# Kernel tuning notes

Hardware: AMD Instinct MI355X
Metric: run time of the kernel (lower is better)

Reference implementation:

```python
import jax, jax.numpy as jnp
import numpy as np

N_NODES = 100000
N_EDGES = 1600000


def setup_inputs() -> dict:
    key = jax.random.key(0)
    ks = jax.random.split(key, 6)
    x = jax.random.normal(ks[0], (N_NODES, 128), dtype=jnp.float32)
    edge_src = jax.random.randint(ks[1], (N_EDGES,), 0, N_NODES, dtype=jnp.int64)
    edge_dst = jax.random.randint(ks[2], (N_EDGES,), 0, N_NODES, dtype=jnp.int64)
    # GCNConv weights (bias=False); glorot-like scaling
    W1 = jax.random.normal(ks[3], (128, 64), dtype=jnp.float32) * (1.0 / np.sqrt(128))
    W2 = jax.random.normal(ks[4], (64, 64), dtype=jnp.float32) * (1.0 / np.sqrt(64))
    W3 = jax.random.normal(ks[5], (64, 40), dtype=jnp.float32) * (1.0 / np.sqrt(64))
    return {"x": x, "edge_src": edge_src, "edge_dst": edge_dst,
            "W1": W1, "W2": W2, "W3": W3}


def reference(x, edge_src, edge_dst, W1, W2, W3):
    # SGC forward (eval mode: dropout is identity).
    # Each GCNConv(normalize=False, bias=False): out = A @ (h @ W)
    n = x.shape[0]

    def conv(h, W):
        hw = h @ W                      # [N, d_out] dense transform
        msgs = hw[edge_src]             # [E, d_out] gather over edges
        return jax.ops.segment_sum(msgs, edge_dst, num_segments=n)  # scatter-add

    h = conv(x, W1)
    h = conv(h, W2)
    h = conv(h, W3)
    return jax.nn.log_softmax(h, axis=-1)
```

## Files before the change

### kernel.cpp

```cpp
#include <hip/hip_runtime.h>
#include <hip/hip_fp16.h>
#include <math.h>


#define BW    128
#define NBMAX 1024
#define BCAP  3072
#define D     40
#define RS    64
#define NPW   12

typedef unsigned short u16;
typedef unsigned int   u32;

static __device__ inline u32 hadd2u(u32 a, u32 b) {
    __half2 ha = *(__half2*)&a, hb = *(__half2*)&b;
    __half2 r = __hadd2(ha, hb);
    return *(u32*)&r;
}

__global__ void k_w12(const float* __restrict__ W1, const float* __restrict__ W2,
                      float* __restrict__ W12, int* __restrict__ gcnt) {
    int idx = blockIdx.x * blockDim.x + threadIdx.x;
    if (blockIdx.x == 0) {
        for (int i = threadIdx.x; i < NBMAX; i += blockDim.x) gcnt[i] = 0;
    }
    if (idx >= 128 * 64) return;
    int r = idx >> 6, c = idx & 63;
    float acc = 0.f;
#pragma unroll
    for (int k = 0; k < 64; ++k) acc += W1[r * 64 + k] * W2[k * 64 + c];
    W12[idx] = acc;
}

__global__ void k_wc(const float* __restrict__ W12, const float* __restrict__ W3,
                     float* __restrict__ Wc) {
    int idx = blockIdx.x * blockDim.x + threadIdx.x;
    if (idx >= 128 * 40) return;
    int r = idx / 40, c = idx - r * 40;
    float acc = 0.f;
#pragma unroll
    for (int k = 0; k < 64; ++k) acc += W12[r * 64 + k] * W3[k * 40 + c];
    Wc[idx] = acc;
}

__global__ void k_gemm(const float4* __restrict__ x4, const float4* __restrict__ Wc4,
                       u16* __restrict__ yout, int n_nodes) {
    __shared__ float4 wc[128 * 10];
    for (int i = threadIdx.x; i < 1280; i += blockDim.x) wc[i] = Wc4[i];
    __syncthreads();
    int tid = blockIdx.x * blockDim.x + threadIdx.x;
    int node = tid / 5, j0 = tid - node * 5;
    if (node >= n_nodes) return;
    float4 a0 = {0.f, 0.f, 0.f, 0.f}, a1 = {0.f, 0.f, 0.f, 0.f};
    const float4* xr = x4 + (size_t)node * 32;
#pragma unroll
    for (int k4 = 0; k4 < 32; ++k4) {
        float4 v = xr[k4];
#pragma unroll
        for (int kk = 0; kk < 4; ++kk) {
            float c = (kk == 0) ? v.x : (kk == 1) ? v.y : (kk == 2) ? v.z : v.w;
            float4 w0 = wc[(k4 * 4 + kk) * 10 + j0 * 2];
            float4 w1 = wc[(k4 * 4 + kk) * 10 + j0 * 2 + 1];
            a0.x += c * w0.x; a0.y += c * w0.y; a0.z += c * w0.z; a0.w += c * w0.w;
            a1.x += c * w1.x; a1.y += c * w1.y; a1.z += c * w1.z; a1.w += c * w1.w;
        }
    }
    __half2 h0 = __floats2half2_rn(a0.x, a0.y);
    __half2 h1 = __floats2half2_rn(a0.z, a0.w);
    __half2 h2 = __floats2half2_rn(a1.x, a1.y);
    __half2 h3 = __floats2half2_rn(a1.z, a1.w);
    uint4 st;
    st.x = *(u32*)&h0; st.y = *(u32*)&h1; st.z = *(u32*)&h2; st.w = *(u32*)&h3;
    *(uint4*)(yout + (size_t)node * RS + j0 * 8) = st;
}

#define PCHUNK 2048
__global__ void k_part(const int* __restrict__ src, const int* __restrict__ dst,
                       int* __restrict__ gcnt, int* __restrict__ part,
                       int E, int nb) {
    __shared__ int h[NBMAX];
    __shared__ int base[NBMAX];
    int t = threadIdx.x;
    int e0 = blockIdx.x * PCHUNK;
    int e1 = min(e0 + PCHUNK, E);
    for (int i = t; i < nb; i += 256) h[i] = 0;
    __syncthreads();
    for (int e = e0 + t; e < e1; e += 256)
        atomicAdd(&h[dst[e] >> 7], 1);
    __syncthreads();
    for (int i = t; i < nb; i += 256) {
        int c = h[i];
        base[i] = c ? atomicAdd(&gcnt[i], c) : 0;
    }
    __syncthreads();
    for (int i = t; i < nb; i += 256) h[i] = 0;
    __syncthreads();
    for (int e = e0 + t; e < e1; e += 1024) {
        bool v1 = (e + 256) < e1, v2 = (e + 512) < e1, v3 = (e + 768) < e1;
        int d0 = dst[e], s0 = src[e];
        int d1 = v1 ? dst[e + 256] : 0, s1 = v1 ? src[e + 256] : 0;
        int d2 = v2 ? dst[e + 512] : 0, s2 = v2 ? src[e + 512] : 0;
        int d3 = v3 ? dst[e + 768] : 0, s3 = v3 ? src[e + 768] : 0;
        int b0 = d0 >> 7, b1 = d1 >> 7, b2 = d2 >> 7, b3 = d3 >> 7;
        int p0 = base[b0] + atomicAdd(&h[b0], 1);
        int p1 = v1 ? (base[b1] + atomicAdd(&h[b1], 1)) : BCAP;
        int p2 = v2 ? (base[b2] + atomicAdd(&h[b2], 1)) : BCAP;
        int p3 = v3 ? (base[b3] + atomicAdd(&h[b3], 1)) : BCAP;
        if (p0 < BCAP) part[(size_t)b0 * BCAP + p0] = (s0 << 7) | (d0 & 127);
        if (p1 < BCAP) part[(size_t)b1 * BCAP + p1] = (s1 << 7) | (d1 & 127);
        if (p2 < BCAP) part[(size_t)b2 * BCAP + p2] = (s2 << 7) | (d2 & 127);
        if (p3 < BCAP) part[(size_t)b3 * BCAP + p3] = (s3 << 7) | (d3 & 127);
    }
}

__global__ void k_csr(const int* __restrict__ part, const int* __restrict__ gcnt,
                      int* __restrict__ begv, int* __restrict__ endv,
                      int* __restrict__ ssort, int N) {
    __shared__ int cnt[BW];
    __shared__ int pos[BW];
    __shared__ int cur[BW];
    __shared__ int wsum[2];
    int b = blockIdx.x, t = threadIdx.x;
    int m = min(gcnt[b], BCAP);
    const int* bp = part + (size_t)b * BCAP;
    if (t < BW) cnt[t] = 0;
    __syncthreads();
    for (int k = t; k < m; k += 256)
        atomicAdd(&cnt[bp[k] & 127], 1);
    __syncthreads();
    int v = 0, inc = 0;
    if (t < BW) {
        v = cnt[t];
        inc = v;
#pragma unroll
        for (int off = 1; off < 64; off <<= 1) {
            int u = __shfl_up(inc, off, 64);
            if ((t & 63) >= off) inc += u;
        }
        if ((t & 63) == 63) wsum[t >> 6] = inc;
    }
    __syncthreads();
    int node0 = b * BW;
    if (t < BW) {
        int local = ((t >= 64) ? wsum[0] : 0) + inc - v;
        pos[t] = local;
        cur[t] = 0;
        if (node0 + t < N) {
            begv[node0 + t] = b * BCAP + local;
            endv[node0 + t] = b * BCAP + local + v;
        }
    }
    __syncthreads();
    for (int k = t; k < m; k += 256) {
        int p = bp[k];
        int r = p & 127;
        int loc = atomicAdd(&cur[r], 1);
        ssort[(size_t)b * BCAP + pos[r] + loc] = p >> 7;
    }
}

template <int FINAL>
__global__ void k_agg(const u16* __restrict__ yin, void* __restrict__ youtv,
                      const int* __restrict__ begv, const int* __restrict__ endv,
                      const int* __restrict__ srcs, int n_nodes) {
    int wid = (blockIdx.x * blockDim.x + threadIdx.x) >> 6;
    int lane = threadIdx.x & 63;
    int g = lane / 5;
    int sub = lane - g * 5;
    int node = wid * NPW + g;
    bool nv = (g < NPW) && (node < n_nodes);
    int ncl = nv ? node : 0;
    int beg = begv[ncl];
    int deg = nv ? (endv[ncl] - beg) : 0;
    u32 suboff = (u32)sub * 16u;
    u32 c0 = 0, c1 = 0, c2 = 0, c3 = 0;
    for (int k = 0; __any(k < deg); k += 5) {
        int sv = (k + sub < deg) ? srcs[beg + k + sub] : 0;
#pragma unroll
        for (int j = 0; j < 5; ++j) {
            int s = __shfl(sv, g * 5 + j, 64);
            if (k + j < deg) {
                uint4 w = *(const uint4*)((const char*)yin +
                              (size_t)(((u32)s << 7) + suboff));
                c0 = hadd2u(c0, w.x); c1 = hadd2u(c1, w.y);
                c2 = hadd2u(c2, w.z); c3 = hadd2u(c3, w.w);
            }
        }
    }
    if (FINAL) {
        float2 f0 = __half22float2(*(__half2*)&c0);
        float2 f1 = __half22float2(*(__half2*)&c1);
        float2 f2 = __half22float2(*(__half2*)&c2);
        float2 f3 = __half22float2(*(__half2*)&c3);
        int s1 = sub + 1; s1 = (s1 >= 5) ? s1 - 5 : s1;
        int s2 = sub + 2; s2 = (s2 >= 5) ? s2 - 5 : s2;
        int s4 = sub + 4; s4 = (s4 >= 5) ? s4 - 5 : s4;
        int r1 = g * 5 + s1, r2 = g * 5 + s2, r4 = g * 5 + s4;
        float m0 = fmaxf(fmaxf(fmaxf(f0.x, f0.y), fmaxf(f1.x, f1.y)),
                         fmaxf(fmaxf(f2.x, f2.y), fmaxf(f3.x, f3.y)));
        float m = fmaxf(m0, __shfl(m0, r1, 64));
        m = fmaxf(m, __shfl(m, r2, 64));
        m = fmaxf(m, __shfl(m0, r4, 64));
        float e0 = __expf(f0.x - m) + __expf(f0.y - m) + __expf(f1.x - m) +
                   __expf(f1.y - m) + __expf(f2.x - m) + __expf(f2.y - m) +
                   __expf(f3.x - m) + __expf(f3.y - m);
        float sm = e0 + __shfl(e0, r1, 64);
        sm = sm + __shfl(sm, r2, 64);
        sm = sm + __shfl(e0, r4, 64);
        float ls = __logf(sm) + m;
        if (nv) {
            float4 o1 = {f0.x - ls, f0.y - ls, f1.x - ls, f1.y - ls};
            float4 o2 = {f2.x - ls, f2.y - ls, f3.x - ls, f3.y - ls};
            float* op = (float*)youtv + (size_t)node * D + sub * 8;
            *(float4*)op = o1;
            *(float4*)(op + 4) = o2;
        }
    } else {
        if (nv) {
            uint4 st = {c0, c1, c2, c3};
            *(uint4*)((u16*)youtv + (size_t)node * RS + sub * 8) = st;
        }
    }
}

extern "C" void kernel_launch(void* const* d_in, const int* in_sizes, int n_in,
                              void* d_out, int out_size, void* d_ws, size_t ws_size,
                              hipStream_t stream) {
    const float* x   = (const float*)d_in[0];
    const int* esrc  = (const int*)d_in[1];
    const int* edst  = (const int*)d_in[2];
    const float* W1  = (const float*)d_in[3];
    const float* W2  = (const float*)d_in[4];
    const float* W3  = (const float*)d_in[5];
    int N = in_sizes[0] / 128;
    int E = in_sizes[1];
    float* out = (float*)d_out;

    int nb = (N + BW - 1) / BW;

    char* ws = (char*)d_ws;
    auto alloc = [&](size_t bytes) {
        char* p = ws;
        ws += (bytes + 255) & ~(size_t)255;
        return p;
    };
    u16* bufA   = (u16*)alloc((size_t)N * RS * sizeof(u16));
    u16* bufB   = (u16*)alloc((size_t)N * RS * sizeof(u16));
    int* part   = (int*)bufB;
    int* ssort  = (int*)alloc((size_t)nb * BCAP * sizeof(int));
    int* begv   = (int*)alloc((size_t)N * sizeof(int));
    int* endv   = (int*)alloc((size_t)N * sizeof(int));
    float* W12  = (float*)alloc(128 * 64 * sizeof(float));
    float* Wc   = (float*)alloc(128 * 40 * sizeof(float));
    int* gcnt   = (int*)alloc(NBMAX * sizeof(int));

    k_w12<<<(128 * 64 + 255) / 256, 256, 0, stream>>>(W1, W2, W12, gcnt);
    k_wc<<<(128 * 40 + 255) / 256, 256, 0, stream>>>(W12, W3, Wc);
    k_gemm<<<(N * 5 + 255) / 256, 256, 0, stream>>>((const float4*)x, (const float4*)Wc,
                                                    bufA, N);

    k_part<<<(E + PCHUNK - 1) / PCHUNK, 256, 0, stream>>>(esrc, edst, gcnt, part, E, nb);
    k_csr<<<nb, 256, 0, stream>>>(part, gcnt, begv, endv, ssort, N);

    int nwaves = (N + NPW - 1) / NPW;
    int agg_grid = (nwaves + 3) / 4;
    k_agg<0><<<agg_grid, 256, 0, stream>>>(bufA, bufB, begv, endv, ssort, N);
    k_agg<0><<<agg_grid, 256, 0, stream>>>(bufB, bufA, begv, endv, ssort, N);
    k_agg<1><<<agg_grid, 256, 0, stream>>>(bufA, out, begv, endv, ssort, N);
}
```

Measured before the change: 195.7 us.

## Fuse GEMM and edge partition into one launch; pack CSR offsets as int2

Merges the dense transform kernel and the edge-bucketing kernel into a single launch. Low block indices do the partition and the rest do the GEMM, sharing LDS through a union, so the two independent stages can run concurrently and one launch is removed. The partition chunk size doubles, and the scatter loop now batches eight edge loads before its atomics. Begin and end offsets are stored as one int2 so the aggregation kernels need a single load per node. Larger chunks mean fewer partition blocks and more LDS-atomic contention per block.

```diff
diff --git a/kernel.cpp b/kernel.cpp
--- a/kernel.cpp
+++ b/kernel.cpp
@@ -9,6 +9,7 @@
 #define D     40
 #define RS    64
 #define NPW   12
+#define PCHUNK 4096
 
 typedef unsigned short u16;
 typedef unsigned int   u32;
@@ -44,79 +45,91 @@
     Wc[idx] = acc;
 }
 
-__global__ void k_gemm(const float4* __restrict__ x4, const float4* __restrict__ Wc4,
-                       u16* __restrict__ yout, int n_nodes) {
-    __shared__ float4 wc[128 * 10];
-    for (int i = threadIdx.x; i < 1280; i += blockDim.x) wc[i] = Wc4[i];
-    __syncthreads();
-    int tid = blockIdx.x * blockDim.x + threadIdx.x;
-    int node = tid / 5, j0 = tid - node * 5;
-    if (node >= n_nodes) return;
-    float4 a0 = {0.f, 0.f, 0.f, 0.f}, a1 = {0.f, 0.f, 0.f, 0.f};
-    const float4* xr = x4 + (size_t)node * 32;
-#pragma unroll
-    for (int k4 = 0; k4 < 32; ++k4) {
-        float4 v = xr[k4];
-#pragma unroll
-        for (int kk = 0; kk < 4; ++kk) {
-            float c = (kk == 0) ? v.x : (kk == 1) ? v.y : (kk == 2) ? v.z : v.w;
-            float4 w0 = wc[(k4 * 4 + kk) * 10 + j0 * 2];
-            float4 w1 = wc[(k4 * 4 + kk) * 10 + j0 * 2 + 1];
-            a0.x += c * w0.x; a0.y += c * w0.y; a0.z += c * w0.z; a0.w += c * w0.w;
-            a1.x += c * w1.x; a1.y += c * w1.y; a1.z += c * w1.z; a1.w += c * w1.w;
-        }
-    }
-    __half2 h0 = __floats2half2_rn(a0.x, a0.y);
-    __half2 h1 = __floats2half2_rn(a0.z, a0.w);
-    __half2 h2 = __floats2half2_rn(a1.x, a1.y);
-    __half2 h3 = __floats2half2_rn(a1.z, a1.w);
-    uint4 st;
-    st.x = *(u32*)&h0; st.y = *(u32*)&h1; st.z = *(u32*)&h2; st.w = *(u32*)&h3;
-    *(uint4*)(yout + (size_t)node * RS + j0 * 8) = st;
-}
-
-#define PCHUNK 2048
-__global__ void k_part(const int* __restrict__ src, const int* __restrict__ dst,
-                       int* __restrict__ gcnt, int* __restrict__ part,
-                       int E, int nb) {
-    __shared__ int h[NBMAX];
-    __shared__ int base[NBMAX];
+__global__ void k_gp(const float4* __restrict__ x4, const float4* __restrict__ Wc4,
+                     u16* __restrict__ yout, int n_nodes,
+                     const int* __restrict__ src, const int* __restrict__ dst,
+                     int* __restrict__ gcnt, int* __restrict__ part,
+                     int E, int nb, int npart) {
+    __shared__ union {
+        struct { int h[NBMAX]; int base[NBMAX]; } p;
+        float4 wc[1280];
+    } sm;
     int t = threadIdx.x;
-    int e0 = blockIdx.x * PCHUNK;
-    int e1 = min(e0 + PCHUNK, E);
-    for (int i = t; i < nb; i += 256) h[i] = 0;
-    __syncthreads();
-    for (int e = e0 + t; e < e1; e += 256)
-        atomicAdd(&h[dst[e] >> 7], 1);
-    __syncthreads();
-    for (int i = t; i < nb; i += 256) {
-        int c = h[i];
-        base[i] = c ? atomicAdd(&gcnt[i], c) : 0;
-    }
-    __syncthreads();
-    for (int i = t; i < nb; i += 256) h[i] = 0;
-    __syncthreads();
-    for (int e = e0 + t; e < e1; e += 1024) {
-        bool v1 = (e + 256) < e1, v2 = (e + 512) < e1, v3 = (e + 768) < e1;
-        int d0 = dst[e], s0 = src[e];
-        int d1 = v1 ? dst[e + 256] : 0, s1 = v1 ? src[e + 256] : 0;
-        int d2 = v2 ? dst[e + 512] : 0, s2 = v2 ? src[e + 512] : 0;
-        int d3 = v3 ? dst[e + 768] : 0, s3 = v3 ? src[e + 768] : 0;
-        int b0 = d0 >> 7, b1 = d1 >> 7, b2 = d2 >> 7, b3 = d3 >> 7;
-        int p0 = base[b0] + atomicAdd(&h[b0], 1);
-        int p1 = v1 ? (base[b1] + atomicAdd(&h[b1], 1)) : BCAP;
-        int p2 = v2 ? (base[b2] + atomicAdd(&h[b2], 1)) : BCAP;
-        int p3 = v3 ? (base[b3] + atomicAdd(&h[b3], 1)) : BCAP;
-        if (p0 < BCAP) part[(size_t)b0 * BCAP + p0] = (s0 << 7) | (d0 & 127);
-        if (p1 < BCAP) part[(size_t)b1 * BCAP + p1] = (s1 << 7) | (d1 & 127);
-        if (p2 < BCAP) part[(size_t)b2 * BCAP + p2] = (s2 << 7) | (d2 & 127);
-        if (p3 < BCAP) part[(size_t)b3 * BCAP + p3] = (s3 << 7) | (d3 & 127);
+
+    if ((int)blockIdx.x < npart) {
+        int e0 = blockIdx.x * PCHUNK;
+        int e1 = min(e0 + PCHUNK, E);
+        for (int i = t; i < nb; i += 256) sm.p.h[i] = 0;
+        __syncthreads();
+        for (int e = e0 + t; e < e1; e += 1024) {
+#pragma unroll
+            for (int u = 0; u < 4; ++u) {
+                int ee = e + u * 256;
+                if (ee < e1) atomicAdd(&sm.p.h[dst[ee] >> 7], 1);
+            }
+        }
+        __syncthreads();
+        for (int i = t; i < nb; i += 256) {
+            int c = sm.p.h[i];
+            sm.p.base[i] = c ? atomicAdd(&gcnt[i], c) : 0;
+        }
+        __syncthreads();
+        for (int i = t; i < nb; i += 256) sm.p.h[i] = 0;
+        __syncthreads();
+        for (int eb = e0 + t; eb < e1; eb += 2048) {
+            int dd[8], ss[8], pp[8];
+#pragma unroll
+            for (int u = 0; u < 8; ++u) {
+                int e = eb + u * 256;
+                bool v = e < e1;
+                dd[u] = v ? dst[e] : 0;
+                ss[u] = v ? src[e] : 0;
+            }
+#pragma unroll
+            for (int u = 0; u < 8; ++u) {
+                int e = eb + u * 256;
+                int b = dd[u] >> 7;
+                pp[u] = (e < e1) ? (sm.p.base[b] + atomicAdd(&sm.p.h[b], 1)) : BCAP;
+            }
+#pragma unroll
+            for (int u = 0; u < 8; ++u) {
+                int b = dd[u] >> 7;
+                if (pp[u] < BCAP)
+                    part[(size_t)b * BCAP + pp[u]] = (ss[u] << 7) | (dd[u] & 127);
+            }
+        }
+    } else {
+        for (int i = t; i < 1280; i += 256) sm.wc[i] = Wc4[i];
+        __syncthreads();
+        int tid = ((int)blockIdx.x - npart) * 256 + t;
+        int node = tid / 5, j0 = tid - node * 5;
+        if (node >= n_nodes) return;
+        float4 a0 = {0.f, 0.f, 0.f, 0.f}, a1 = {0.f, 0.f, 0.f, 0.f};
+        const float4* xr = x4 + (size_t)node * 32;
+#pragma unroll
+        for (int k4 = 0; k4 < 32; ++k4) {
+            float4 v = xr[k4];
+#pragma unroll
+            for (int kk = 0; kk < 4; ++kk) {
+                float c = (kk == 0) ? v.x : (kk == 1) ? v.y : (kk == 2) ? v.z : v.w;
+                float4 w0 = sm.wc[(k4 * 4 + kk) * 10 + j0 * 2];
+                float4 w1 = sm.wc[(k4 * 4 + kk) * 10 + j0 * 2 + 1];
+                a0.x += c * w0.x; a0.y += c * w0.y; a0.z += c * w0.z; a0.w += c * w0.w;
+                a1.x += c * w1.x; a1.y += c * w1.y; a1.z += c * w1.z; a1.w += c * w1.w;
+            }
+        }
+        __half2 h0 = __floats2half2_rn(a0.x, a0.y);
+        __half2 h1 = __floats2half2_rn(a0.z, a0.w);
+        __half2 h2 = __floats2half2_rn(a1.x, a1.y);
+        __half2 h3 = __floats2half2_rn(a1.z, a1.w);
+        uint4 st;
+        st.x = *(u32*)&h0; st.y = *(u32*)&h1; st.z = *(u32*)&h2; st.w = *(u32*)&h3;
+        *(uint4*)(yout + (size_t)node * RS + j0 * 8) = st;
     }
 }
 
 __global__ void k_csr(const int* __restrict__ part, const int* __restrict__ gcnt,
-                      int* __restrict__ begv, int* __restrict__ endv,
-                      int* __restrict__ ssort, int N) {
+                      int2* __restrict__ offs2, int* __restrict__ ssort, int N) {
     __shared__ int cnt[BW];
     __shared__ int pos[BW];
     __shared__ int cur[BW];
@@ -146,10 +159,8 @@
         int local = ((t >= 64) ? wsum[0] : 0) + inc - v;
         pos[t] = local;
         cur[t] = 0;
-        if (node0 + t < N) {
-            begv[node0 + t] = b * BCAP + local;
-            endv[node0 + t] = b * BCAP + local + v;
-        }
+        if (node0 + t < N)
+            offs2[node0 + t] = make_int2(b * BCAP + local, b * BCAP + local + v);
     }
     __syncthreads();
     for (int k = t; k < m; k += 256) {
@@ -162,17 +173,17 @@
 
 template <int FINAL>
 __global__ void k_agg(const u16* __restrict__ yin, void* __restrict__ youtv,
-                      const int* __restrict__ begv, const int* __restrict__ endv,
-                      const int* __restrict__ srcs, int n_nodes) {
+                      const int2* __restrict__ offs2, const int* __restrict__ srcs,
+                      int n_nodes) {
     int wid = (blockIdx.x * blockDim.x + threadIdx.x) >> 6;
     int lane = threadIdx.x & 63;
     int g = lane / 5;
     int sub = lane - g * 5;
     int node = wid * NPW + g;
     bool nv = (g < NPW) && (node < n_nodes);
-    int ncl = nv ? node : 0;
-    int beg = begv[ncl];
-    int deg = nv ? (endv[ncl] - beg) : 0;
+    int2 be = offs2[nv ? node : 0];
+    int beg = be.x;
+    int deg = nv ? (be.y - be.x) : 0;
     u32 suboff = (u32)sub * 16u;
     u32 c0 = 0, c1 = 0, c2 = 0, c3 = 0;
     for (int k = 0; __any(k < deg); k += 5) {
@@ -249,23 +260,25 @@
     u16* bufB   = (u16*)alloc((size_t)N * RS * sizeof(u16));
     int* part   = (int*)bufB;
     int* ssort  = (int*)alloc((size_t)nb * BCAP * sizeof(int));
-    int* begv   = (int*)alloc((size_t)N * sizeof(int));
-    int* endv   = (int*)alloc((size_t)N * sizeof(int));
+    int2* offs2 = (int2*)alloc((size_t)N * sizeof(int2));
     float* W12  = (float*)alloc(128 * 64 * sizeof(float));
     float* Wc   = (float*)alloc(128 * 40 * sizeof(float));
     int* gcnt   = (int*)alloc(NBMAX * sizeof(int));
 
     k_w12<<<(128 * 64 + 255) / 256, 256, 0, stream>>>(W1, W2, W12, gcnt);
     k_wc<<<(128 * 40 + 255) / 256, 256, 0, stream>>>(W12, W3, Wc);
-    k_gemm<<<(N * 5 + 255) / 256, 256, 0, stream>>>((const float4*)x, (const float4*)Wc,
-                                                    bufA, N);
-
-    k_part<<<(E + PCHUNK - 1) / PCHUNK, 256, 0, stream>>>(esrc, edst, gcnt, part, E, nb);
-    k_csr<<<nb, 256, 0, stream>>>(part, gcnt, begv, endv, ssort, N);
+
+    int npart = (E + PCHUNK - 1) / PCHUNK;
+    int ngemm = (N * 5 + 255) / 256;
+    k_gp<<<npart + ngemm, 256, 0, stream>>>((const float4*)x, (const float4*)Wc,
+                                            bufA, N, esrc, edst, gcnt, part,
+                                            E, nb, npart);
+
+    k_csr<<<nb, 256, 0, stream>>>(part, gcnt, offs2, ssort, N);
 
     int nwaves = (N + NPW - 1) / NPW;
     int agg_grid = (nwaves + 3) / 4;
-    k_agg<0><<<agg_grid, 256, 0, stream>>>(bufA, bufB, begv, endv, ssort, N);
-    k_agg<0><<<agg_grid, 256, 0, stream>>>(bufB, bufA, begv, endv, ssort, N);
-    k_agg<1><<<agg_grid, 256, 0, stream>>>(bufA, out, begv, endv, ssort, N);
-}
+    k_agg<0><<<agg_grid, 256, 0, stream>>>(bufA, bufB, offs2, ssort, N);
+    k_agg<0><<<agg_grid, 256, 0, stream>>>(bufB, bufA, offs2, ssort, N);
+    k_agg<1><<<agg_grid, 256, 0, stream>>>(bufA, out, offs2, ssort, N);
+}
```

Result: faster. 174.2 us (median of 2 runs) (-11.0%).
